# Kernel tuning notes

Measured on AMD Instinct MI355X. Metric: run time of the kernel, lower is better.

Reference implementation:

```python
import jax, jax.numpy as jnp
import numpy as np

NUM_HEADS = 32
NUM_FEATURES = 512
CPH = NUM_FEATURES // NUM_HEADS  # 16


def _grouped_1x1(x_flat, w, b, groups):
    # x_flat: (B, Cin); w: (Cout, Cin//groups); b: (Cout,)
    B, Cin = x_flat.shape
    Cout = w.shape[0]
    xg = x_flat.reshape(B, groups, Cin // groups)
    wg = w.reshape(groups, Cout // groups, Cin // groups)
    out = jnp.einsum('bgi,goi->bgo', xg, wg).reshape(B, Cout) + b
    return out


def _attend(x, w, b):
    # x: (B, C, H, W, Z) zero-mean input; w: (num_heads, CPH); b: (num_heads,)
    B, C, H, W, Z = x.shape
    N = H * W * Z
    xr = x.reshape(B, NUM_HEADS, CPH, N)
    # grouped 1x1 conv producing one attention logit map per head
    logits = jnp.einsum('bhcn,hc->bhn', xr, w) + b[None, :, None]
    attn = jax.nn.softmax(logits, axis=-1)  # softmax over spatial
    res = jnp.einsum('bhcn,bhn->bhc', xr, attn)  # weighted pooling
    return res.reshape(B, C, 1, 1, 1)


def setup_inputs() -> dict:
    key = jax.random.key(0)
    ks = jax.random.split(key, 7)
    C = NUM_FEATURES
    x = jax.random.normal(ks[0], (4, C, 32, 32, 32), dtype=jnp.float32)
    # P module: conv1 C->C/2 groups=32, conv2 C/2->C groups=32 (kaiming-like scale)
    pw1 = jax.random.normal(ks[1], (C // 2, C // NUM_HEADS), dtype=jnp.float32) * np.float32(np.sqrt(2.0 / (C // 2)))
    pb1 = jnp.zeros((C // 2,), dtype=jnp.float32)
    pw2 = jax.random.normal(ks[2], (C, (C // 2) // NUM_HEADS), dtype=jnp.float32) * np.float32(np.sqrt(2.0 / C))
    pb2 = jnp.zeros((C,), dtype=jnp.float32)
    kw = jax.random.normal(ks[3], (NUM_HEADS, CPH), dtype=jnp.float32) * np.float32(np.sqrt(2.0 / NUM_HEADS))
    kb = jnp.zeros((NUM_HEADS,), dtype=jnp.float32)
    qw = jax.random.normal(ks[4], (NUM_HEADS, CPH), dtype=jnp.float32) * np.float32(np.sqrt(2.0 / NUM_HEADS))
    qb = jnp.zeros((NUM_HEADS,), dtype=jnp.float32)
    return {"x": x, "pw1": pw1, "pb1": pb1, "pw2": pw2, "pb2": pb2,
            "kw": kw, "kb": kb, "qw": qw, "qb": qb}


def reference(x, pw1, pb1, pw2, pb2, kw, kb, qw, qb):
    B, C, H, W, Z = x.shape
    mu = x.mean(axis=(2, 3, 4), keepdims=True)  # (B,C,1,1,1)
    x_mu = x - mu
    # P: grouped bottleneck MLP on mu with sigmoid gate
    h1 = jax.nn.relu(_grouped_1x1(mu.reshape(B, C), pw1, pb1, NUM_HEADS))
    P = jax.nn.sigmoid(_grouped_1x1(h1, pw2, pb2, NUM_HEADS)).reshape(B, C, 1, 1, 1)
    K = _attend(x_mu, kw, kb)
    Q = _attend(x_mu, qw, qb)
    y = (x + K - Q) * P
    dp = jnp.mean(K * Q, axis=1, keepdims=True)  # (B,1,1,1,1)
    return (y, dp)
```

## Files before the change

kernel.cpp:

```cpp
#include <hip/hip_runtime.h>
#include <math.h>

namespace {

constexpr int B = 4;
constexpr int C = 512;
constexpr int NH = 32;
constexpr int CPH = 16;
constexpr int N = 32 * 32 * 32;
constexpr int NJ = 32;
constexpr int NREC = NJ * 4;
constexpr long YSIZE = (long)B * C * N;

typedef float f4v __attribute__((ext_vector_type(4)));

__device__ inline float wrs(float v) {
#pragma unroll
  for (int o = 32; o > 0; o >>= 1) v += __shfl_xor(v, o);
  return v;
}

template <int CTRL, int RM = 0xF>
__device__ __forceinline__ float dppAdd(float v) {
  const int r = __builtin_amdgcn_update_dpp(
      0, __float_as_int(v), CTRL, RM, 0xF, true);
  return v + __int_as_float(r);
}
__device__ __forceinline__ float waveSumRow3(float v) {
  v = dppAdd<0xB1>(v);
  v = dppAdd<0x4E>(v);
  v = dppAdd<0x124>(v);
  v = dppAdd<0x128>(v);
  v = dppAdd<0x142, 0xA>(v);
  v = dppAdd<0x143, 0xC>(v);
  return v;
}

__global__ __launch_bounds__(256, 4) void kA(const float* __restrict__ x,
                                             const float* __restrict__ kw,
                                             const float* __restrict__ qw,
                                             float* __restrict__ prec) {
  const int b = blockIdx.z, h = blockIdx.y, j = blockIdx.x;
  const int t = threadIdx.x, lane = t & 63, wid = t >> 6;
  const int p = lane & 15;
  const float* xs = x + ((long)(b * C + h * CPH)) * N + (long)j * 1024 + t * 4;

  float4 xv[CPH];
#pragma unroll
  for (int c = 0; c < CPH; ++c) xv[c] = *(const float4*)(xs + (long)c * N);

  float4 lk = make_float4(0.f, 0.f, 0.f, 0.f);
  float4 lq = make_float4(0.f, 0.f, 0.f, 0.f);
#pragma unroll
  for (int c = 0; c < CPH; ++c) {
    const float wkc = kw[h * CPH + c], wqc = qw[h * CPH + c];
    lk.x += xv[c].x * wkc; lk.y += xv[c].y * wkc;
    lk.z += xv[c].z * wkc; lk.w += xv[c].w * wkc;
    lq.x += xv[c].x * wqc; lq.y += xv[c].y * wqc;
    lq.z += xv[c].z * wqc; lq.w += xv[c].w * wqc;
  }
  const float4 ek = make_float4(__expf(lk.x), __expf(lk.y),
                                __expf(lk.z), __expf(lk.w));
  const float4 eq = make_float4(__expf(lq.x), __expf(lq.y),
                                __expf(lq.z), __expf(lq.w));
  const float sK = waveSumRow3((ek.x + ek.y) + (ek.z + ek.w));
  const float sQ = waveSumRow3((eq.x + eq.y) + (eq.z + eq.w));

  float o0 = 0.f, o1 = 0.f, o2 = 0.f;
#pragma unroll
  for (int c = 0; c < CPH; ++c) {
    float dk = (xv[c].x * ek.x + xv[c].y * ek.y) + (xv[c].z * ek.z + xv[c].w * ek.w);
    float dq = (xv[c].x * eq.x + xv[c].y * eq.y) + (xv[c].z * eq.z + xv[c].w * eq.w);
    float cs = (xv[c].x + xv[c].y) + (xv[c].z + xv[c].w);
    dk = waveSumRow3(dk);
    dq = waveSumRow3(dq);
    cs = waveSumRow3(cs);
    if (p == c) { o0 = dk; o1 = dq; o2 = cs; }
  }
  const float o3 = (p == 0) ? sK : ((p == 1) ? sQ : 0.f);

  if ((lane >> 4) == 3) {
    const long ridx = (((long)(b * NH + h)) * NJ + j) * 4 + wid;
    f4v r; r.x = o0; r.y = o1; r.z = o2; r.w = o3;
    *(f4v*)(prec + ridx * 64 + p * 4) = r;
  }
}

__global__ __launch_bounds__(512) void k4(const float* __restrict__ prec,
                                          const float* __restrict__ pw1,
                                          const float* __restrict__ pb1,
                                          const float* __restrict__ pw2,
                                          const float* __restrict__ pb2,
                                          float* __restrict__ scale,
                                          float* __restrict__ offset,
                                          float* __restrict__ dpOut) {
  const int b = blockIdx.x;
  const int c = threadIdx.x;
  const int h = c >> 4, i = c & 15;
  const float4* rec4 = (const float4*)prec + ((long)(b * NH + h)) * NREC * 16;

  float dk = 0.f, dq = 0.f, cs = 0.f, sacc = 0.f;
  for (int j = 0; j < NREC; ++j) {
    const float4 r = rec4[j * 16 + i];
    dk += r.x; dq += r.y; cs += r.z; sacc += r.w;
  }
  __shared__ float skS[NH], sqS[NH];
  if (i == 0) skS[h] = sacc;
  if (i == 1) sqS[h] = sacc;
  __syncthreads();
  const float sk = skS[h], sq = sqS[h];

  const float mu = cs * (1.f / N);
  const float Kv = dk / sk - mu;
  const float Qv = dq / sq - mu;

  __shared__ float muS[C], h1S[256];
  muS[c] = mu;
  __syncthreads();
  if (c < 256) {
    const int g = c >> 3;
    float a = pb1[c];
#pragma unroll
    for (int k = 0; k < 16; ++k) a += muS[g * 16 + k] * pw1[c * 16 + k];
    h1S[c] = fmaxf(a, 0.f);
  }
  __syncthreads();
  float a = pb2[c];
  const int g2 = c >> 4;
#pragma unroll
  for (int k = 0; k < 8; ++k) a += h1S[g2 * 8 + k] * pw2[c * 8 + k];
  const float P = 1.f / (1.f + __expf(-a));
  scale[b * C + c] = P;
  offset[b * C + c] = (Kv - Qv) * P;

  float pdp = wrs(Kv * Qv);
  __shared__ float pS[8];
  const int lane = c & 63, wid = c >> 6;
  if (lane == 0) pS[wid] = pdp;
  __syncthreads();
  if (c == 0) {
    float tot = 0.f;
    for (int w = 0; w < 8; ++w) tot += pS[w];
    dpOut[b] = tot * (1.f / C);
  }
}

__global__ __launch_bounds__(256) void k5(const float* __restrict__ x,
                                          const float* __restrict__ scale,
                                          const float* __restrict__ offset,
                                          float* __restrict__ y) {
  const int b = blockIdx.z, cc = blockIdx.y;
  const int t = threadIdx.x;
  const long base = ((long)(b * C + cc)) * N + (long)blockIdx.x * 4096;
  const float s = scale[b * C + cc], o = offset[b * C + cc];
#pragma unroll
  for (int k = 0; k < 4; ++k) {
    const long i = base + (long)(k * 256 + t) * 4;
    const float4 v = *(const float4*)(x + i);
    f4v w;
    w.x = v.x * s + o; w.y = v.y * s + o;
    w.z = v.z * s + o; w.w = v.w * s + o;
    __builtin_nontemporal_store(w, (f4v*)(y + i));
  }
}

}

extern "C" void kernel_launch(void* const* d_in, const int* in_sizes, int n_in,
                              void* d_out, int out_size, void* d_ws, size_t ws_size,
                              hipStream_t stream) {
  const float* x   = (const float*)d_in[0];
  const float* pw1 = (const float*)d_in[1];
  const float* pb1 = (const float*)d_in[2];
  const float* pw2 = (const float*)d_in[3];
  const float* pb2 = (const float*)d_in[4];
  const float* kw  = (const float*)d_in[5];
  const float* qw  = (const float*)d_in[7];
  float* out = (float*)d_out;
  float* ws  = (float*)d_ws;

  float* scale  = ws;
  float* offset = ws + 2048;

  constexpr long PREC = (long)B * NH * NREC * 64;
  float* prec;
  if (ws_size >= (size_t)(4096 + PREC) * sizeof(float)) {
    prec = ws + 4096;
  } else {
    prec = out;
  }

  hipLaunchKernelGGL(kA, dim3(NJ, NH, B), dim3(256), 0, stream,
                     x, kw, qw, prec);
  hipLaunchKernelGGL(k4, dim3(B), dim3(C), 0, stream,
                     prec, pw1, pb1, pw2, pb2, scale, offset, out + YSIZE);
  hipLaunchKernelGGL(k5, dim3(N / 4096, C, B), dim3(256), 0, stream,
                     x, scale, offset, out);
}
```

Measured before the change: 144.3 us.

## Fuse stats, gating and output into one cooperative kernel with per-head sync

Replaces the three-kernel pipeline with a single cooperative kernel. Each block reduces softmax statistics for its slice of a head, then waits on a per-head atomic counter. After that it computes the gating MLP and K/Q locally and writes y from its own slice, re-reading it in reverse order to improve cache hits. This removes the intermediate launches and the separate k4 kernel, and may reduce DRAM traffic on the second read of x. It adds spin-wait synchronisation, two memsets and a co-residency requirement.

```diff
diff --git a/kernel.cpp b/kernel.cpp
--- a/kernel.cpp
+++ b/kernel.cpp
@@ -8,6 +8,8 @@
 constexpr int NH = 32;
 constexpr int CPH = 16;
 constexpr int N = 32 * 32 * 32;
+constexpr int JG = 8;
+constexpr int CPB = 4;
 constexpr int NJ = 32;
 constexpr int NREC = NJ * 4;
 constexpr long YSIZE = (long)B * C * N;
@@ -36,6 +38,126 @@
   return v;
 }
 
+__global__ __launch_bounds__(256, 4) void fused(
+    const float* __restrict__ x, const float* __restrict__ kw,
+    const float* __restrict__ qw, const float* __restrict__ pw1,
+    const float* __restrict__ pb1, const float* __restrict__ pw2,
+    const float* __restrict__ pb2, float* __restrict__ prec,
+    int* __restrict__ cnt, float* __restrict__ dp, float* __restrict__ y) {
+  const int jg = blockIdx.x, h = blockIdx.y, b = blockIdx.z;
+  const int t = threadIdx.x, lane = t & 63, wid = t >> 6, p = lane & 15;
+  const int head = b * NH + h;
+  const float* xh = x + ((long)(b * C + h * CPH)) * N;
+
+  float o0 = 0.f, o1 = 0.f, o2 = 0.f, o3 = 0.f;
+  for (int s = 0; s < CPB; ++s) {
+    const float* xs = xh + (long)(jg * CPB + s) * 1024 + t * 4;
+    float4 xv[CPH];
+#pragma unroll
+    for (int c = 0; c < CPH; ++c) xv[c] = *(const float4*)(xs + (long)c * N);
+    float4 lk = make_float4(0.f, 0.f, 0.f, 0.f);
+    float4 lq = make_float4(0.f, 0.f, 0.f, 0.f);
+#pragma unroll
+    for (int c = 0; c < CPH; ++c) {
+      const float wk = kw[h * CPH + c], wq = qw[h * CPH + c];
+      lk.x += xv[c].x * wk; lk.y += xv[c].y * wk;
+      lk.z += xv[c].z * wk; lk.w += xv[c].w * wk;
+      lq.x += xv[c].x * wq; lq.y += xv[c].y * wq;
+      lq.z += xv[c].z * wq; lq.w += xv[c].w * wq;
+    }
+    const float4 ek = make_float4(__expf(lk.x), __expf(lk.y),
+                                  __expf(lk.z), __expf(lk.w));
+    const float4 eq = make_float4(__expf(lq.x), __expf(lq.y),
+                                  __expf(lq.z), __expf(lq.w));
+    const float sK = waveSumRow3((ek.x + ek.y) + (ek.z + ek.w));
+    const float sQ = waveSumRow3((eq.x + eq.y) + (eq.z + eq.w));
+    o3 += (p == 0) ? sK : ((p == 1) ? sQ : 0.f);
+#pragma unroll
+    for (int c = 0; c < CPH; ++c) {
+      float dk = (xv[c].x * ek.x + xv[c].y * ek.y) + (xv[c].z * ek.z + xv[c].w * ek.w);
+      float dq = (xv[c].x * eq.x + xv[c].y * eq.y) + (xv[c].z * eq.z + xv[c].w * eq.w);
+      float cs = (xv[c].x + xv[c].y) + (xv[c].z + xv[c].w);
+      dk = waveSumRow3(dk);
+      dq = waveSumRow3(dq);
+      cs = waveSumRow3(cs);
+      if (p == c) { o0 += dk; o1 += dq; o2 += cs; }
+    }
+  }
+  float* rec = prec + ((long)head * 32 + jg * 4 + wid) * 64;
+  if ((lane >> 4) == 3) {
+    rec[p] = o0; rec[16 + p] = o1; rec[32 + p] = o2; rec[48 + p] = o3;
+  }
+  __syncthreads();
+  __threadfence();
+  if (t == 0)
+    __hip_atomic_fetch_add(&cnt[head], 1, __ATOMIC_RELEASE,
+                           __HIP_MEMORY_SCOPE_AGENT);
+  if (lane == 0) {
+    while (__hip_atomic_load(&cnt[head], __ATOMIC_RELAXED,
+                             __HIP_MEMORY_SCOPE_AGENT) < JG)
+      __builtin_amdgcn_s_sleep(8);
+  }
+  __syncthreads();
+  (void)__hip_atomic_load(&cnt[head], __ATOMIC_ACQUIRE,
+                          __HIP_MEMORY_SCOPE_AGENT);
+
+  const float* recs = prec + (long)head * 32 * 64;
+  float v = 0.f;
+#pragma unroll 8
+  for (int r = 0; r < 32; ++r) v += recs[r * 64 + lane];
+
+  __shared__ float slotS[64], muS[CPH], h1S[8], KvS[CPH], QvS[CPH],
+      scS[CPH], ofS[CPH];
+  if (wid == 0) slotS[lane] = v;
+  __syncthreads();
+  if (t < CPH) {
+    const float sk = slotS[48], sq = slotS[49];
+    const float mu = slotS[32 + t] * (1.f / N);
+    muS[t] = mu;
+    KvS[t] = slotS[t] / sk - mu;
+    QvS[t] = slotS[16 + t] / sq - mu;
+  }
+  __syncthreads();
+  if (t < 8) {
+    float a = pb1[h * 8 + t];
+#pragma unroll
+    for (int i = 0; i < 16; ++i) a += muS[i] * pw1[(h * 8 + t) * 16 + i];
+    h1S[t] = fmaxf(a, 0.f);
+  }
+  __syncthreads();
+  if (t < CPH) {
+    float a = pb2[h * 16 + t];
+#pragma unroll
+    for (int k = 0; k < 8; ++k) a += h1S[k] * pw2[(h * 16 + t) * 8 + k];
+    const float P = 1.f / (1.f + __expf(-a));
+    scS[t] = P;
+    ofS[t] = (KvS[t] - QvS[t]) * P;
+  }
+  __syncthreads();
+  if (jg == 0 && t == 0) {
+    float sdp = 0.f;
+#pragma unroll
+    for (int c2 = 0; c2 < CPH; ++c2) sdp += KvS[c2] * QvS[c2];
+    atomicAdd(&dp[b], sdp * (1.f / C));
+  }
+
+  float* yh = y + ((long)(b * C + h * CPH)) * N;
+  for (int s = CPB - 1; s >= 0; --s) {
+    const long off = (long)(jg * CPB + s) * 1024 + t * 4;
+    float4 xv[CPH];
+#pragma unroll
+    for (int c = 0; c < CPH; ++c) xv[c] = *(const float4*)(xh + off + (long)c * N);
+#pragma unroll
+    for (int c = 0; c < CPH; ++c) {
+      const float sc = scS[c], of = ofS[c];
+      f4v w;
+      w.x = xv[c].x * sc + of; w.y = xv[c].y * sc + of;
+      w.z = xv[c].z * sc + of; w.w = xv[c].w * sc + of;
+      __builtin_nontemporal_store(w, (f4v*)(yh + off + (long)c * N));
+    }
+  }
+}
+
 __global__ __launch_bounds__(256, 4) void kA(const float* __restrict__ x,
                                              const float* __restrict__ kw,
                                              const float* __restrict__ qw,
@@ -44,11 +166,9 @@
   const int t = threadIdx.x, lane = t & 63, wid = t >> 6;
   const int p = lane & 15;
   const float* xs = x + ((long)(b * C + h * CPH)) * N + (long)j * 1024 + t * 4;
-
   float4 xv[CPH];
 #pragma unroll
   for (int c = 0; c < CPH; ++c) xv[c] = *(const float4*)(xs + (long)c * N);
-
   float4 lk = make_float4(0.f, 0.f, 0.f, 0.f);
   float4 lq = make_float4(0.f, 0.f, 0.f, 0.f);
 #pragma unroll
@@ -65,20 +185,16 @@
                                 __expf(lq.z), __expf(lq.w));
   const float sK = waveSumRow3((ek.x + ek.y) + (ek.z + ek.w));
   const float sQ = waveSumRow3((eq.x + eq.y) + (eq.z + eq.w));
-
   float o0 = 0.f, o1 = 0.f, o2 = 0.f;
 #pragma unroll
   for (int c = 0; c < CPH; ++c) {
     float dk = (xv[c].x * ek.x + xv[c].y * ek.y) + (xv[c].z * ek.z + xv[c].w * ek.w);
     float dq = (xv[c].x * eq.x + xv[c].y * eq.y) + (xv[c].z * eq.z + xv[c].w * eq.w);
     float cs = (xv[c].x + xv[c].y) + (xv[c].z + xv[c].w);
-    dk = waveSumRow3(dk);
-    dq = waveSumRow3(dq);
-    cs = waveSumRow3(cs);
+    dk = waveSumRow3(dk); dq = waveSumRow3(dq); cs = waveSumRow3(cs);
     if (p == c) { o0 = dk; o1 = dq; o2 = cs; }
   }
   const float o3 = (p == 0) ? sK : ((p == 1) ? sQ : 0.f);
-
   if ((lane >> 4) == 3) {
     const long ridx = (((long)(b * NH + h)) * NJ + j) * 4 + wid;
     f4v r; r.x = o0; r.y = o1; r.z = o2; r.w = o3;
@@ -98,7 +214,6 @@
   const int c = threadIdx.x;
   const int h = c >> 4, i = c & 15;
   const float4* rec4 = (const float4*)prec + ((long)(b * NH + h)) * NREC * 16;
-
   float dk = 0.f, dq = 0.f, cs = 0.f, sacc = 0.f;
   for (int j = 0; j < NREC; ++j) {
     const float4 r = rec4[j * 16 + i];
@@ -109,11 +224,9 @@
   if (i == 1) sqS[h] = sacc;
   __syncthreads();
   const float sk = skS[h], sq = sqS[h];
-
   const float mu = cs * (1.f / N);
   const float Kv = dk / sk - mu;
   const float Qv = dq / sq - mu;
-
   __shared__ float muS[C], h1S[256];
   muS[c] = mu;
   __syncthreads();
@@ -132,7 +245,6 @@
   const float P = 1.f / (1.f + __expf(-a));
   scale[b * C + c] = P;
   offset[b * C + c] = (Kv - Qv) * P;
-
   float pdp = wrs(Kv * Qv);
   __shared__ float pS[8];
   const int lane = c & 63, wid = c >> 6;
@@ -179,21 +291,36 @@
   float* out = (float*)d_out;
   float* ws  = (float*)d_ws;
 
-  float* scale  = ws;
-  float* offset = ws + 2048;
-
-  constexpr long PREC = (long)B * NH * NREC * 64;
-  float* prec;
-  if (ws_size >= (size_t)(4096 + PREC) * sizeof(float)) {
-    prec = ws + 4096;
-  } else {
-    prec = out;
-  }
-
-  hipLaunchKernelGGL(kA, dim3(NJ, NH, B), dim3(256), 0, stream,
-                     x, kw, qw, prec);
-  hipLaunchKernelGGL(k4, dim3(B), dim3(C), 0, stream,
-                     prec, pw1, pb1, pw2, pb2, scale, offset, out + YSIZE);
-  hipLaunchKernelGGL(k5, dim3(N / 4096, C, B), dim3(256), 0, stream,
-                     x, scale, offset, out);
-}
+  constexpr long FPREC = (long)B * NH * 32 * 64;
+  const bool wsOK = ws_size >= (size_t)(4096 + FPREC) * sizeof(float);
+
+  bool launched = false;
+  if (wsOK) {
+    int* cnt = (int*)ws;
+    float* prec = ws + 4096;
+    float* dpp = out + YSIZE;
+    float* yp = out;
+    hipMemsetAsync(ws, 0, B * NH * sizeof(int), stream);
+    hipMemsetAsync(dpp, 0, B * sizeof(float), stream);
+    void* args[] = {(void*)&x,   (void*)&kw,  (void*)&qw,  (void*)&pw1,
+                    (void*)&pb1, (void*)&pw2, (void*)&pb2, (void*)&prec,
+                    (void*)&cnt, (void*)&dpp, (void*)&yp};
+    const hipError_t e = hipLaunchCooperativeKernel(
+        (const void*)fused, dim3(JG, NH, B), dim3(256), args, 0, stream);
+    launched = (e == hipSuccess);
+  }
+
+  if (!launched) {
+    float* scale  = ws;
+    float* offset = ws + 2048;
+    constexpr long PREC = (long)B * NH * NREC * 64;
+    float* prec = (ws_size >= (size_t)(4096 + PREC) * sizeof(float))
+                      ? (ws + 4096) : out;
+    hipLaunchKernelGGL(kA, dim3(NJ, NH, B), dim3(256), 0, stream,
+                       x, kw, qw, prec);
+    hipLaunchKernelGGL(k4, dim3(B), dim3(C), 0, stream,
+                       prec, pw1, pb1, pw2, pb2, scale, offset, out + YSIZE);
+    hipLaunchKernelGGL(k5, dim3(N / 4096, C, B), dim3(256), 0, stream,
+                       x, scale, offset, out);
+  }
+}
```

Result: slower. 394.2 us (+173.2%).
